# Performance work log

Measured on AMD Instinct MI355X. Metric: run time of the kernel, lower is better.

The kernel has to match this reference:

```python
import jax, jax.numpy as jnp
import numpy as np

N_NODES = 50000
N_EDGES = 800000
IN_CH = 384
HID = 128


def _gcn_conv(x, src, dst, W, b, n):
    # PyG GCNConv: h = x @ W; out[dst] += d^-1/2[src] * d^-1/2[dst] * h[src]; out += b
    h = x @ W  # [N, out_ch]
    deg = jax.ops.segment_sum(jnp.ones(src.shape, dtype=h.dtype), dst, num_segments=n)
    dinv = jnp.where(deg > 0, jax.lax.rsqrt(jnp.maximum(deg, 1.0)), 0.0)
    norm = dinv[src] * dinv[dst]  # [E]
    out = jax.ops.segment_sum(h[src] * norm[:, None], dst, num_segments=n)
    return out + b


def setup_inputs() -> dict:
    key = jax.random.key(0)
    k_x, k_e, k1, k2, k3, k4 = jax.random.split(key, 6)
    x = jax.random.normal(k_x, (N_NODES, IN_CH), dtype=jnp.float32)
    edge_index = jax.random.randint(k_e, (2, N_EDGES), 0, N_NODES, dtype=jnp.int64)
    s1 = 1.0 / np.sqrt(IN_CH)
    s2 = 1.0 / np.sqrt(HID)
    W1 = jax.random.uniform(k1, (IN_CH, HID), jnp.float32, -s1, s1)
    b1 = jnp.zeros((HID,), jnp.float32)
    W2 = jax.random.uniform(k2, (HID, HID), jnp.float32, -s2, s2)
    b2 = jnp.zeros((HID,), jnp.float32)
    return {"x": x, "edge_index": edge_index, "W1": W1, "b1": b1, "W2": W2, "b2": b2}


def reference(x, edge_index, W1, b1, W2, b2):
    n = x.shape[0]
    loops = jnp.arange(n, dtype=edge_index.dtype)
    src = jnp.concatenate([edge_index[0], loops])  # add_self_loops
    dst = jnp.concatenate([edge_index[1], loops])
    h = _gcn_conv(x, src, dst, W1, b1, n)
    h = jax.nn.relu(h)  # dropout is identity in eval mode
    out = _gcn_conv(h, src, dst, W2, b2, n)
    return out
```

## Files before the change

### kernel.cpp

```cpp
#include <hip/hip_runtime.h>
#include <hip/hip_fp16.h>

#define NN 50000
#define NE 800000
#define C_IN 384
#define C_HID 128
#define NB 196
#define CHK 128
#define ECH 6250
#define NBKT 128
#define BSTR 392

typedef __attribute__((ext_vector_type(8))) short short8;
typedef __attribute__((ext_vector_type(4))) float f32x4;
typedef __attribute__((ext_vector_type(4))) unsigned short us4;

__device__ __forceinline__ ushort f2bf(float x) {
    uint u = __float_as_uint(x);
    uint r = (u + 0x7fffu + ((u >> 16) & 1u)) >> 16;
    return (ushort)r;
}
__device__ __forceinline__ float bf2f(ushort b) { return __uint_as_float(((uint)b) << 16); }

__global__ __launch_bounds__(256) void k_dinv(const int* __restrict__ cnt,
                                              float* __restrict__ dinv) {
    int i = blockIdx.x * 256 + threadIdx.x;
    if (i < NN) dinv[i] = rsqrtf((float)cnt[i] + 1.0f);
}

__global__ __launch_bounds__(256) void k_bsum(const int* __restrict__ cnt,
                                              int* __restrict__ bsum) {
    __shared__ int part[256];
    const int tid = threadIdx.x;
    const int i = blockIdx.x * 256 + tid;
    part[tid] = (i < NN) ? cnt[i] : 0;
    __syncthreads();
#pragma unroll
    for (int off = 128; off > 0; off >>= 1) {
        if (tid < off) part[tid] += part[tid + off];
        __syncthreads();
    }
    if (tid == 0) bsum[blockIdx.x] = part[0];
}

__global__ __launch_bounds__(256) void k_sbs(const int* __restrict__ bsum,
                                             int* __restrict__ bpre) {
    __shared__ int part[256];
    const int t = threadIdx.x;
    part[t] = (t < NB) ? bsum[t] : 0;
    __syncthreads();
#pragma unroll
    for (int off = 1; off < 256; off <<= 1) {
        int v = (t >= off) ? part[t - off] : 0;
        __syncthreads();
        part[t] += v;
        __syncthreads();
    }
    if (t < NB) bpre[t] = (t == 0) ? 0 : part[t - 1];
}

__global__ __launch_bounds__(256) void k_write(const int* __restrict__ cnt,
                                               const int* __restrict__ bpre,
                                               int* __restrict__ rowptr) {
    __shared__ int part[256];
    const int t = threadIdx.x;
    const int i = blockIdx.x * 256 + t;
    const int v = (i < NN) ? cnt[i] : 0;
    part[t] = v;
    __syncthreads();
#pragma unroll
    for (int off = 1; off < 256; off <<= 1) {
        int u = (t >= off) ? part[t - off] : 0;
        __syncthreads();
        part[t] += u;
        __syncthreads();
    }
    if (i < NN) {
        const int excl = bpre[blockIdx.x] + part[t] - v;
        rowptr[i] = excl;
        if (i == NN - 1) rowptr[NN] = excl + v;
    }
}

__global__ __launch_bounds__(256) void k_hist(const int* __restrict__ dst,
                                              int* __restrict__ histT) {
    __shared__ int h[NBKT];
    const int tid = threadIdx.x;
    if (tid < NBKT) h[tid] = 0;
    __syncthreads();
    const int base = blockIdx.x * ECH;
    for (int i = base + tid; i < base + ECH; i += 256)
        atomicAdd(&h[(uint)dst[i] / BSTR], 1);
    __syncthreads();
    if (tid < NBKT) histT[tid * CHK + blockIdx.x] = h[tid];
}

__global__ __launch_bounds__(1024) void k_hscan(const int* __restrict__ histT,
                                                int* __restrict__ histS) {
    __shared__ int part[1024];
    const int t = threadIdx.x;
    const int base = t * 16;
    int loc[16];
    int s = 0;
#pragma unroll
    for (int i = 0; i < 16; ++i) {
        loc[i] = histT[base + i];
        s += loc[i];
    }
    part[t] = s;
    __syncthreads();
    for (int off = 1; off < 1024; off <<= 1) {
        int v = (t >= off) ? part[t - off] : 0;
        __syncthreads();
        part[t] += v;
        __syncthreads();
    }
    int run = (t == 0) ? 0 : part[t - 1];
#pragma unroll
    for (int i = 0; i < 16; ++i) {
        histS[base + i] = run;
        run += loc[i];
    }
}

__global__ __launch_bounds__(256) void k_binscat(const int* __restrict__ src,
                                                 const int* __restrict__ dst,
                                                 const int* __restrict__ histS,
                                                 uint2* __restrict__ mid) {
    __shared__ int cur[NBKT];
    const int tid = threadIdx.x;
    if (tid < NBKT) cur[tid] = histS[tid * CHK + blockIdx.x];
    __syncthreads();
    const int base = blockIdx.x * ECH;
    for (int i = base + tid; i < base + ECH; i += 256) {
        const int s = src[i];
        const int d = dst[i];
        const int p = atomicAdd(&cur[(uint)d / BSTR], 1);
        mid[p] = make_uint2((uint)d, (uint)s << 16);
    }
}

__global__ __launch_bounds__(256) void k_bcnt(const uint2* __restrict__ mid,
                                              const int* __restrict__ histS,
                                              int* __restrict__ cnt) {
    __shared__ int cur[BSTR];
    const int tid = threadIdx.x;
    const int b = blockIdx.x;
    for (int j = tid; j < BSTR; j += 256) cur[j] = 0;
    __syncthreads();
    const int lo = histS[b * CHK];
    const int hi = (b < NBKT - 1) ? histS[(b + 1) * CHK] : NE;
    for (int e = lo + tid; e < hi; e += 256)
        atomicAdd(&cur[mid[e].x - (uint)b * BSTR], 1);
    __syncthreads();
    for (int j = tid; j < BSTR; j += 256) {
        const int idx = b * BSTR + j;
        if (idx < NN) cnt[idx] = cur[j];
    }
}

__global__ __launch_bounds__(256) void k_binfill(const uint2* __restrict__ mid,
                                                 const int* __restrict__ histS,
                                                 const int* __restrict__ rowptr,
                                                 const float* __restrict__ dinv,
                                                 uint* __restrict__ csr) {
    __shared__ int cur[BSTR];
    __shared__ float sdv[BSTR];
    const int tid = threadIdx.x;
    const int b = blockIdx.x;
    for (int j = tid; j < BSTR; j += 256) {
        const int idx = b * BSTR + j;
        cur[j] = (idx < NN) ? rowptr[idx] : 0;
        sdv[j] = (idx < NN) ? dinv[idx] : 0.f;
    }
    __syncthreads();
    const int lo = histS[b * CHK];
    const int hi = (b < NBKT - 1) ? histS[(b + 1) * CHK] : NE;
    for (int e = lo + tid; e < hi; e += 256) {
        const uint2 u = mid[e];
        const int j = u.x - (uint)b * BSTR;
        const float norm = dinv[u.y >> 16] * sdv[j];
        const int p = atomicAdd(&cur[j], 1);
        csr[p] = u.y | __half_as_ushort(__float2half(norm));
    }
}

__global__ __launch_bounds__(256) void k_wconv(const float* __restrict__ W,
                                               ushort* __restrict__ Wt,
                                               int K) {
    int i = blockIdx.x * 256 + threadIdx.x;
    if (i < K * C_HID) {
        int k = i >> 7, n = i & 127;
        float w = W[i];
        ushort h = f2bf(w);
        ushort l = f2bf(w - bf2f(h));
        int blk = k >> 6, khalf = (k >> 5) & 1, kq = (k >> 3) & 3, j = k & 7;
        int t = n >> 4, fr = n & 15, lane = kq * 16 + fr;
        size_t off = (size_t)blk * 16384 + (size_t)((khalf * 8 + t) * 64 + lane) * 8 + j;
        Wt[off] = h;
        Wt[off + 8192] = l;
    }
}

template <bool IN_RELU_BIAS, bool OUT_BIAS>
__global__ __launch_bounds__(256, 4) void k_gemm_mfma(const float* __restrict__ X,
                                                      const ushort* __restrict__ Wt,
                                                      const float* __restrict__ bin,
                                                      const float* __restrict__ bout,
                                                      const float* __restrict__ dinv,
                                                      ushort* __restrict__ out_main,
                                                      float* __restrict__ out_self,
                                                      int K) {
    const int tid = threadIdx.x;
    const int bm = blockIdx.x * 32;
    const int wv = tid >> 6;
    const int lane = tid & 63;
    const int fr = lane & 15;
    const int kq = lane >> 4;
    const int g = wv >> 1;
    const int ch = wv & 1;

    int row = bm + g * 16 + fr;
    if (row >= NN) row = NN - 1;
    const float* xrow = X + (size_t)row * K + kq * 8;
    const short8* Wt8 = (const short8*)Wt;

    f32x4 acc[4];
#pragma unroll
    for (int t = 0; t < 4; ++t) acc[t] = (f32x4){0.f, 0.f, 0.f, 0.f};

    float4 xa0 = *(const float4*)(xrow);
    float4 xa1 = *(const float4*)(xrow + 4);
    float4 xb0 = *(const float4*)(xrow + 32);
    float4 xb1 = *(const float4*)(xrow + 36);

    for (int k0 = 0; k0 < K; k0 += 64) {
        const short8* gB = Wt8 + (size_t)(k0 >> 6) * 2048;
        short8 b_h0[4], b_l0[4], b_h1[4], b_l1[4];
#pragma unroll
        for (int t = 0; t < 4; ++t) {
            const int tt = ch * 4 + t;
            b_h0[t] = gB[tt * 64 + lane];
            b_l0[t] = gB[1024 + tt * 64 + lane];
            b_h1[t] = gB[(8 + tt) * 64 + lane];
            b_l1[t] = gB[1024 + (8 + tt) * 64 + lane];
        }

        float xv[16] = {xa0.x, xa0.y, xa0.z, xa0.w, xa1.x, xa1.y, xa1.z, xa1.w,
                        xb0.x, xb0.y, xb0.z, xb0.w, xb1.x, xb1.y, xb1.z, xb1.w};
        if (IN_RELU_BIAS) {
            const float* bp = bin + k0 + kq * 8;
            float4 b0 = *(const float4*)(bp);
            float4 b1 = *(const float4*)(bp + 4);
            float4 b2 = *(const float4*)(bp + 32);
            float4 b3 = *(const float4*)(bp + 36);
            const float bb[16] = {b0.x, b0.y, b0.z, b0.w, b1.x, b1.y, b1.z, b1.w,
                                  b2.x, b2.y, b2.z, b2.w, b3.x, b3.y, b3.z, b3.w};
#pragma unroll
            for (int j = 0; j < 16; ++j) xv[j] = fmaxf(xv[j] + bb[j], 0.f);
        }
        union { ushort u[8]; short8 v; } ah0, al0, ah1, al1;
#pragma unroll
        for (int j = 0; j < 8; ++j) {
            uint u = __float_as_uint(xv[j]);
            ah0.u[j] = (ushort)(u >> 16);
            al0.u[j] = (ushort)(__float_as_uint(xv[j] - __uint_as_float(u & 0xffff0000u)) >> 16);
            uint w = __float_as_uint(xv[8 + j]);
            ah1.u[j] = (ushort)(w >> 16);
            al1.u[j] = (ushort)(__float_as_uint(xv[8 + j] - __uint_as_float(w & 0xffff0000u)) >> 16);
        }

        if (k0 + 64 < K) {
            const float* ap = xrow + k0 + 64;
            xa0 = *(const float4*)(ap);
            xa1 = *(const float4*)(ap + 4);
            xb0 = *(const float4*)(ap + 32);
            xb1 = *(const float4*)(ap + 36);
        }

#pragma unroll
        for (int t = 0; t < 4; ++t) {
            acc[t] = __builtin_amdgcn_mfma_f32_16x16x32_bf16(ah0.v, b_h0[t], acc[t], 0, 0, 0);
            acc[t] = __builtin_amdgcn_mfma_f32_16x16x32_bf16(ah0.v, b_l0[t], acc[t], 0, 0, 0);
            acc[t] = __builtin_amdgcn_mfma_f32_16x16x32_bf16(al0.v, b_h0[t], acc[t], 0, 0, 0);
            acc[t] = __builtin_amdgcn_mfma_f32_16x16x32_bf16(ah1.v, b_h1[t], acc[t], 0, 0, 0);
            acc[t] = __builtin_amdgcn_mfma_f32_16x16x32_bf16(ah1.v, b_l1[t], acc[t], 0, 0, 0);
            acc[t] = __builtin_amdgcn_mfma_f32_16x16x32_bf16(al1.v, b_h1[t], acc[t], 0, 0, 0);
        }
    }

#pragma unroll
    for (int r = 0; r < 4; ++r) {
        const int m = bm + g * 16 + kq * 4 + r;
        if (m < NN) {
            const float dv = dinv[m];
            const float d2 = dv * dv;
            ushort* om = out_main + (size_t)m * C_HID;
            float* os = out_self + (size_t)m * C_HID;
#pragma unroll
            for (int t = 0; t < 4; ++t) {
                const int n = (ch * 4 + t) * 16 + fr;
                const float v = acc[t][r];
                om[n] = f2bf(v);
                os[n] = v * d2 + (OUT_BIAS ? bout[n] : 0.f);
            }
        }
    }
}

__global__ __launch_bounds__(256) void k_gather(const ushort* __restrict__ h,
                                                const int* __restrict__ rowptr,
                                                const uint* __restrict__ csr,
                                                float* __restrict__ out) {
    const int tid = threadIdx.x;
    const int node = blockIdx.x * 8 + (tid >> 5);
    if (node >= NN) return;
    const int lane = tid & 31;
    const int c = lane * 4;
    const int beg = rowptr[node];
    const int end = rowptr[node + 1];

    float4 acc = *(const float4*)(out + (size_t)node * C_HID + c);

    for (int j0 = beg; j0 < end; j0 += 32) {
        const int n = end - j0;
        uint myE = 0;
        if (lane < n) myE = csr[j0 + lane];
        const int m = n < 32 ? n : 32;
        int jj = 0;
        for (; jj + 4 <= m; jj += 4) {
            const uint e0 = (uint)__shfl((int)myE, jj + 0, 32);
            const uint e1 = (uint)__shfl((int)myE, jj + 1, 32);
            const uint e2 = (uint)__shfl((int)myE, jj + 2, 32);
            const uint e3 = (uint)__shfl((int)myE, jj + 3, 32);
            const us4 u0 = *(const us4*)(h + (size_t)(e0 >> 16) * C_HID + c);
            const us4 u1 = *(const us4*)(h + (size_t)(e1 >> 16) * C_HID + c);
            const us4 u2 = *(const us4*)(h + (size_t)(e2 >> 16) * C_HID + c);
            const us4 u3 = *(const us4*)(h + (size_t)(e3 >> 16) * C_HID + c);
            const float n0 = __half2float(__ushort_as_half((ushort)(e0 & 0xffffu)));
            const float n1 = __half2float(__ushort_as_half((ushort)(e1 & 0xffffu)));
            const float n2 = __half2float(__ushort_as_half((ushort)(e2 & 0xffffu)));
            const float n3 = __half2float(__ushort_as_half((ushort)(e3 & 0xffffu)));
            acc.x = fmaf(bf2f(u0[0]), n0, acc.x);
            acc.y = fmaf(bf2f(u0[1]), n0, acc.y);
            acc.z = fmaf(bf2f(u0[2]), n0, acc.z);
            acc.w = fmaf(bf2f(u0[3]), n0, acc.w);
            acc.x = fmaf(bf2f(u1[0]), n1, acc.x);
            acc.y = fmaf(bf2f(u1[1]), n1, acc.y);
            acc.z = fmaf(bf2f(u1[2]), n1, acc.z);
            acc.w = fmaf(bf2f(u1[3]), n1, acc.w);
            acc.x = fmaf(bf2f(u2[0]), n2, acc.x);
            acc.y = fmaf(bf2f(u2[1]), n2, acc.y);
            acc.z = fmaf(bf2f(u2[2]), n2, acc.z);
            acc.w = fmaf(bf2f(u2[3]), n2, acc.w);
            acc.x = fmaf(bf2f(u3[0]), n3, acc.x);
            acc.y = fmaf(bf2f(u3[1]), n3, acc.y);
            acc.z = fmaf(bf2f(u3[2]), n3, acc.z);
            acc.w = fmaf(bf2f(u3[3]), n3, acc.w);
        }
        for (; jj < m; ++jj) {
            const uint ev = (uint)__shfl((int)myE, jj, 32);
            const us4 u = *(const us4*)(h + (size_t)(ev >> 16) * C_HID + c);
            const float nw = __half2float(__ushort_as_half((ushort)(ev & 0xffffu)));
            acc.x = fmaf(bf2f(u[0]), nw, acc.x);
            acc.y = fmaf(bf2f(u[1]), nw, acc.y);
            acc.z = fmaf(bf2f(u[2]), nw, acc.z);
            acc.w = fmaf(bf2f(u[3]), nw, acc.w);
        }
    }
    *(float4*)(out + (size_t)node * C_HID + c) = acc;
}

extern "C" void kernel_launch(void* const* d_in, const int* in_sizes, int n_in,
                              void* d_out, int out_size, void* d_ws, size_t ws_size,
                              hipStream_t stream) {
    const float* x = (const float*)d_in[0];
    const int* ei = (const int*)d_in[1];
    const float* W1 = (const float*)d_in[2];
    const float* b1 = (const float*)d_in[3];
    const float* W2 = (const float*)d_in[4];
    const float* b2 = (const float*)d_in[5];
    float* out = (float*)d_out;

    const int* src = ei;
    const int* dst = ei + NE;

    int* cnt = (int*)d_ws;
    int* rowptr = cnt + 50048;
    float* dinv = (float*)(rowptr + 50064);
    int* bsum = (int*)(dinv + 50048);
    int* bpre = bsum + 256;
    int* histT = bpre + 256;
    int* histS = histT + 16384;
    ushort* Wt1 = (ushort*)(histS + 16384);
    ushort* Wt2 = Wt1 + 98304;
    uint* csr = (uint*)(Wt2 + 32768);
    uint2* mid = (uint2*)(csr + NE);
    ushort* A_bf = (ushort*)(mid + NE);
    float* B = (float*)(A_bf + (size_t)NN * C_HID);

    k_wconv<<<(C_IN * C_HID + 255) / 256, 256, 0, stream>>>(W1, Wt1, C_IN);
    k_wconv<<<(C_HID * C_HID + 255) / 256, 256, 0, stream>>>(W2, Wt2, C_HID);
    k_hist<<<CHK, 256, 0, stream>>>(dst, histT);
    k_hscan<<<1, 1024, 0, stream>>>(histT, histS);
    k_binscat<<<CHK, 256, 0, stream>>>(src, dst, histS, mid);
    k_bcnt<<<NBKT, 256, 0, stream>>>(mid, histS, cnt);
    k_dinv<<<NB, 256, 0, stream>>>(cnt, dinv);
    k_bsum<<<NB, 256, 0, stream>>>(cnt, bsum);
    k_sbs<<<1, 256, 0, stream>>>(bsum, bpre);
    k_write<<<NB, 256, 0, stream>>>(cnt, bpre, rowptr);
    k_binfill<<<NBKT, 256, 0, stream>>>(mid, histS, rowptr, dinv, csr);

    const int gblocks = (NN + 31) / 32;
    const int agblocks = (NN + 7) / 8;
    k_gemm_mfma<false, false><<<gblocks, 256, 0, stream>>>(x, Wt1, nullptr, nullptr, dinv, A_bf, B, C_IN);
    k_gather<<<agblocks, 256, 0, stream>>>(A_bf, rowptr, csr, B);
    k_gemm_mfma<true, true><<<gblocks, 256, 0, stream>>>(B, Wt2, b1, b2, dinv, A_bf, out, C_HID);
    k_gather<<<agblocks, 256, 0, stream>>>(A_bf, rowptr, csr, out);
}
```

Before: 354.7 us.

## Stage GEMM weights and activations through double-buffered LDS with async loads

Rewrites the MFMA GEMM to use 512-thread blocks over 64 rows. Weight tiles are loaded asynchronously into double-buffered LDS with global_load_lds, and the X tile goes into swizzled LDS instead of each wave reading global memory directly. The K step shrinks to 32, the weight layout is re-packed to match, and the bias is staged in LDS. The goal is to share weight loads across waves and overlap the next tile's fetch with the MFMA work. The cost is per-step barriers, hand-placed waitcnts whose correctness depends on ordering, and lower occupancy from more LDS use.

```diff
diff --git a/kernel.cpp b/kernel.cpp
--- a/kernel.cpp
+++ b/kernel.cpp
@@ -22,6 +22,12 @@
 }
 __device__ __forceinline__ float bf2f(ushort b) { return __uint_as_float(((uint)b) << 16); }
 
+typedef __attribute__((address_space(1))) const unsigned int as1_uint;
+typedef __attribute__((address_space(3))) unsigned int as3_uint;
+__device__ __forceinline__ void gload16(const void* g, void* l) {
+    __builtin_amdgcn_global_load_lds((as1_uint*)g, (as3_uint*)l, 16, 0, 0);
+}
+
 __global__ __launch_bounds__(256) void k_dinv(const int* __restrict__ cnt,
                                               float* __restrict__ dinv) {
     int i = blockIdx.x * 256 + threadIdx.x;
@@ -194,98 +200,185 @@
         float w = W[i];
         ushort h = f2bf(w);
         ushort l = f2bf(w - bf2f(h));
-        int blk = k >> 6, khalf = (k >> 5) & 1, kq = (k >> 3) & 3, j = k & 7;
+        int blk = k >> 5, kq = (k >> 3) & 3, j = k & 7;
         int t = n >> 4, fr = n & 15, lane = kq * 16 + fr;
-        size_t off = (size_t)blk * 16384 + (size_t)((khalf * 8 + t) * 64 + lane) * 8 + j;
+        size_t off = ((size_t)blk * 1024 + t * 64 + lane) * 8 + j;
         Wt[off] = h;
-        Wt[off + 8192] = l;
-    }
-}
+        Wt[off + 4096] = l;
+    }
+}
+
+#define GEMM_BODY(KB, CUR, NXT, XOLD, XNEW)                                               \
+    {                                                                                     \
+        _Pragma("unroll")                                                                 \
+        for (int i_ = 0; i_ < 2; ++i_)                                                    \
+            gload16(Wt8 + (size_t)((KB) + 1) * 1024 + wv * 128 + i_ * 64 + lane,          \
+                    &WL[NXT][wv * 128 + i_ * 64]);                                        \
+        __builtin_amdgcn_sched_barrier(0);                                                \
+        XNEW = *(const float4*)(xsrc + ((KB) + 2) * 32);                                  \
+        *(float4*)(xdst[NXT]) = XOLD;                                                     \
+        const float* xb_ = &XL[CUR][ar * 32];                                             \
+        float4 xf0 = *(const float4*)(xb_ + ac0);                                         \
+        float4 xf1 = *(const float4*)(xb_ + ac1);                                         \
+        float xv[8] = {xf0.x, xf0.y, xf0.z, xf0.w, xf1.x, xf1.y, xf1.z, xf1.w};           \
+        if (IN_RELU_BIAS) {                                                               \
+            float4 b0 = *(const float4*)(&bias_lds[(KB) * 32 + kq * 8]);                  \
+            float4 b1 = *(const float4*)(&bias_lds[(KB) * 32 + kq * 8 + 4]);              \
+            const float bb[8] = {b0.x, b0.y, b0.z, b0.w, b1.x, b1.y, b1.z, b1.w};         \
+            _Pragma("unroll")                                                             \
+            for (int j_ = 0; j_ < 8; ++j_) xv[j_] = fmaxf(xv[j_] + bb[j_], 0.f);          \
+        }                                                                                 \
+        union { ushort u[8]; short8 v; } ah, al;                                          \
+        _Pragma("unroll")                                                                 \
+        for (int j_ = 0; j_ < 8; ++j_) {                                                  \
+            uint u_ = __float_as_uint(xv[j_]);                                            \
+            ah.u[j_] = (ushort)(u_ >> 16);                                                \
+            al.u[j_] = (ushort)(__float_as_uint(xv[j_] - __uint_as_float(u_ & 0xffff0000u)) >> 16); \
+        }                                                                                 \
+        __builtin_amdgcn_s_setprio(1);                                                    \
+        _Pragma("unroll")                                                                 \
+        for (int t_ = 0; t_ < 4; ++t_) {                                                  \
+            const int tt_ = ch * 4 + t_;                                                  \
+            const short8 wh_ = WL[CUR][tt_ * 64 + lane];                                  \
+            const short8 wl_ = WL[CUR][512 + tt_ * 64 + lane];                            \
+            acc[t_] = __builtin_amdgcn_mfma_f32_16x16x32_bf16(ah.v, wh_, acc[t_], 0, 0, 0); \
+            acc[t_] = __builtin_amdgcn_mfma_f32_16x16x32_bf16(ah.v, wl_, acc[t_], 0, 0, 0); \
+            acc[t_] = __builtin_amdgcn_mfma_f32_16x16x32_bf16(al.v, wh_, acc[t_], 0, 0, 0); \
+        }                                                                                 \
+        __builtin_amdgcn_s_setprio(0);                                                    \
+        __builtin_amdgcn_sched_barrier(0);                                                \
+        asm volatile("s_waitcnt vmcnt(1) lgkmcnt(0)" ::: "memory");                       \
+        __builtin_amdgcn_sched_barrier(0);                                                \
+        __builtin_amdgcn_s_barrier();                                                     \
+    }
 
 template <bool IN_RELU_BIAS, bool OUT_BIAS>
-__global__ __launch_bounds__(256, 4) void k_gemm_mfma(const float* __restrict__ X,
-                                                      const ushort* __restrict__ Wt,
-                                                      const float* __restrict__ bin,
-                                                      const float* __restrict__ bout,
-                                                      const float* __restrict__ dinv,
-                                                      ushort* __restrict__ out_main,
-                                                      float* __restrict__ out_self,
-                                                      int K) {
-    const int tid = threadIdx.x;
-    const int bm = blockIdx.x * 32;
+__global__ __launch_bounds__(512) void k_gemm_mfma(const float* __restrict__ X,
+                                                   const ushort* __restrict__ Wt,
+                                                   const float* __restrict__ bin,
+                                                   const float* __restrict__ bout,
+                                                   const float* __restrict__ dinv,
+                                                   ushort* __restrict__ out_main,
+                                                   float* __restrict__ out_self,
+                                                   int K) {
+    __shared__ short8 WL[2][1024];
+    __shared__ float XL[2][2048];
+    __shared__ float bias_lds[128];
+
+    const int tid = threadIdx.x;
+    const int bm = blockIdx.x * 64;
     const int wv = tid >> 6;
     const int lane = tid & 63;
     const int fr = lane & 15;
     const int kq = lane >> 4;
     const int g = wv >> 1;
     const int ch = wv & 1;
-
-    int row = bm + g * 16 + fr;
-    if (row >= NN) row = NN - 1;
-    const float* xrow = X + (size_t)row * K + kq * 8;
+    const int NK = K >> 5;
+
     const short8* Wt8 = (const short8*)Wt;
 
+    const int xr = tid >> 3;
+    const int xc16 = tid & 7;
+    int xrow = bm + xr;
+    if (xrow >= NN) xrow = NN - 1;
+    const float* xsrc = X + (size_t)xrow * K + xc16 * 4;
+    float* xdst[2] = {&XL[0][xr * 32 + ((xc16 ^ (xr & 7)) * 4)],
+                      &XL[1][xr * 32 + ((xc16 ^ (xr & 7)) * 4)]};
+
+    const int ar = g * 16 + fr;
+    const int ac0 = ((2 * kq) ^ (ar & 7)) * 4;
+    const int ac1 = ((2 * kq + 1) ^ (ar & 7)) * 4;
+
     f32x4 acc[4];
 #pragma unroll
     for (int t = 0; t < 4; ++t) acc[t] = (f32x4){0.f, 0.f, 0.f, 0.f};
 
-    float4 xa0 = *(const float4*)(xrow);
-    float4 xa1 = *(const float4*)(xrow + 4);
-    float4 xb0 = *(const float4*)(xrow + 32);
-    float4 xb1 = *(const float4*)(xrow + 36);
-
-    for (int k0 = 0; k0 < K; k0 += 64) {
-        const short8* gB = Wt8 + (size_t)(k0 >> 6) * 2048;
-        short8 b_h0[4], b_l0[4], b_h1[4], b_l1[4];
-#pragma unroll
-        for (int t = 0; t < 4; ++t) {
-            const int tt = ch * 4 + t;
-            b_h0[t] = gB[tt * 64 + lane];
-            b_l0[t] = gB[1024 + tt * 64 + lane];
-            b_h1[t] = gB[(8 + tt) * 64 + lane];
-            b_l1[t] = gB[1024 + (8 + tt) * 64 + lane];
-        }
-
-        float xv[16] = {xa0.x, xa0.y, xa0.z, xa0.w, xa1.x, xa1.y, xa1.z, xa1.w,
-                        xb0.x, xb0.y, xb0.z, xb0.w, xb1.x, xb1.y, xb1.z, xb1.w};
+    if (IN_RELU_BIAS && tid < 128) bias_lds[tid] = bin[tid];
+
+#pragma unroll
+    for (int i_ = 0; i_ < 2; ++i_)
+        gload16(Wt8 + (size_t)wv * 128 + i_ * 64 + lane, &WL[0][wv * 128 + i_ * 64]);
+    __builtin_amdgcn_sched_barrier(0);
+    float4 xA = *(const float4*)(xsrc);
+    float4 xB = *(const float4*)(xsrc + 32);
+    *(float4*)(xdst[0]) = xA;
+    xA = xB;
+    asm volatile("s_waitcnt lgkmcnt(0)" ::: "memory");
+    __builtin_amdgcn_sched_barrier(0);
+    __builtin_amdgcn_s_barrier();
+
+    for (int kb = 0; kb < NK - 2; kb += 2) {
+        GEMM_BODY(kb, 0, 1, xA, xB);
+        GEMM_BODY(kb + 1, 1, 0, xB, xA);
+    }
+
+    {
+        const int KB = NK - 2;
+#pragma unroll
+        for (int i_ = 0; i_ < 2; ++i_)
+            gload16(Wt8 + (size_t)(KB + 1) * 1024 + wv * 128 + i_ * 64 + lane,
+                    &WL[1][wv * 128 + i_ * 64]);
+        *(float4*)(xdst[1]) = xA;
+        const float* xb_ = &XL[0][ar * 32];
+        float4 xf0 = *(const float4*)(xb_ + ac0);
+        float4 xf1 = *(const float4*)(xb_ + ac1);
+        float xv[8] = {xf0.x, xf0.y, xf0.z, xf0.w, xf1.x, xf1.y, xf1.z, xf1.w};
         if (IN_RELU_BIAS) {
-            const float* bp = bin + k0 + kq * 8;
-            float4 b0 = *(const float4*)(bp);
-            float4 b1 = *(const float4*)(bp + 4);
-            float4 b2 = *(const float4*)(bp + 32);
-            float4 b3 = *(const float4*)(bp + 36);
-            const float bb[16] = {b0.x, b0.y, b0.z, b0.w, b1.x, b1.y, b1.z, b1.w,
-                                  b2.x, b2.y, b2.z, b2.w, b3.x, b3.y, b3.z, b3.w};
-#pragma unroll
-            for (int j = 0; j < 16; ++j) xv[j] = fmaxf(xv[j] + bb[j], 0.f);
-        }
-        union { ushort u[8]; short8 v; } ah0, al0, ah1, al1;
-#pragma unroll
-        for (int j = 0; j < 8; ++j) {
-            uint u = __float_as_uint(xv[j]);
-            ah0.u[j] = (ushort)(u >> 16);
-            al0.u[j] = (ushort)(__float_as_uint(xv[j] - __uint_as_float(u & 0xffff0000u)) >> 16);
-            uint w = __float_as_uint(xv[8 + j]);
-            ah1.u[j] = (ushort)(w >> 16);
-            al1.u[j] = (ushort)(__float_as_uint(xv[8 + j] - __uint_as_float(w & 0xffff0000u)) >> 16);
-        }
-
-        if (k0 + 64 < K) {
-            const float* ap = xrow + k0 + 64;
-            xa0 = *(const float4*)(ap);
-            xa1 = *(const float4*)(ap + 4);
-            xb0 = *(const float4*)(ap + 32);
-            xb1 = *(const float4*)(ap + 36);
-        }
-
-#pragma unroll
-        for (int t = 0; t < 4; ++t) {
-            acc[t] = __builtin_amdgcn_mfma_f32_16x16x32_bf16(ah0.v, b_h0[t], acc[t], 0, 0, 0);
-            acc[t] = __builtin_amdgcn_mfma_f32_16x16x32_bf16(ah0.v, b_l0[t], acc[t], 0, 0, 0);
-            acc[t] = __builtin_amdgcn_mfma_f32_16x16x32_bf16(al0.v, b_h0[t], acc[t], 0, 0, 0);
-            acc[t] = __builtin_amdgcn_mfma_f32_16x16x32_bf16(ah1.v, b_h1[t], acc[t], 0, 0, 0);
-            acc[t] = __builtin_amdgcn_mfma_f32_16x16x32_bf16(ah1.v, b_l1[t], acc[t], 0, 0, 0);
-            acc[t] = __builtin_amdgcn_mfma_f32_16x16x32_bf16(al1.v, b_h1[t], acc[t], 0, 0, 0);
+            float4 b0 = *(const float4*)(&bias_lds[KB * 32 + kq * 8]);
+            float4 b1 = *(const float4*)(&bias_lds[KB * 32 + kq * 8 + 4]);
+            const float bb[8] = {b0.x, b0.y, b0.z, b0.w, b1.x, b1.y, b1.z, b1.w};
+#pragma unroll
+            for (int j_ = 0; j_ < 8; ++j_) xv[j_] = fmaxf(xv[j_] + bb[j_], 0.f);
+        }
+        union { ushort u[8]; short8 v; } ah, al;
+#pragma unroll
+        for (int j_ = 0; j_ < 8; ++j_) {
+            uint u_ = __float_as_uint(xv[j_]);
+            ah.u[j_] = (ushort)(u_ >> 16);
+            al.u[j_] = (ushort)(__float_as_uint(xv[j_] - __uint_as_float(u_ & 0xffff0000u)) >> 16);
+        }
+#pragma unroll
+        for (int t_ = 0; t_ < 4; ++t_) {
+            const int tt_ = ch * 4 + t_;
+            const short8 wh_ = WL[0][tt_ * 64 + lane];
+            const short8 wl_ = WL[0][512 + tt_ * 64 + lane];
+            acc[t_] = __builtin_amdgcn_mfma_f32_16x16x32_bf16(ah.v, wh_, acc[t_], 0, 0, 0);
+            acc[t_] = __builtin_amdgcn_mfma_f32_16x16x32_bf16(ah.v, wl_, acc[t_], 0, 0, 0);
+            acc[t_] = __builtin_amdgcn_mfma_f32_16x16x32_bf16(al.v, wh_, acc[t_], 0, 0, 0);
+        }
+        __builtin_amdgcn_sched_barrier(0);
+        asm volatile("s_waitcnt vmcnt(0) lgkmcnt(0)" ::: "memory");
+        __builtin_amdgcn_sched_barrier(0);
+        __builtin_amdgcn_s_barrier();
+    }
+    {
+        const int KB = NK - 1;
+        const float* xb_ = &XL[1][ar * 32];
+        float4 xf0 = *(const float4*)(xb_ + ac0);
+        float4 xf1 = *(const float4*)(xb_ + ac1);
+        float xv[8] = {xf0.x, xf0.y, xf0.z, xf0.w, xf1.x, xf1.y, xf1.z, xf1.w};
+        if (IN_RELU_BIAS) {
+            float4 b0 = *(const float4*)(&bias_lds[KB * 32 + kq * 8]);
+            float4 b1 = *(const float4*)(&bias_lds[KB * 32 + kq * 8 + 4]);
+            const float bb[8] = {b0.x, b0.y, b0.z, b0.w, b1.x, b1.y, b1.z, b1.w};
+#pragma unroll
+            for (int j_ = 0; j_ < 8; ++j_) xv[j_] = fmaxf(xv[j_] + bb[j_], 0.f);
+        }
+        union { ushort u[8]; short8 v; } ah, al;
+#pragma unroll
+        for (int j_ = 0; j_ < 8; ++j_) {
+            uint u_ = __float_as_uint(xv[j_]);
+            ah.u[j_] = (ushort)(u_ >> 16);
+            al.u[j_] = (ushort)(__float_as_uint(xv[j_] - __uint_as_float(u_ & 0xffff0000u)) >> 16);
+        }
+#pragma unroll
+        for (int t_ = 0; t_ < 4; ++t_) {
+            const int tt_ = ch * 4 + t_;
+            const short8 wh_ = WL[1][tt_ * 64 + lane];
+            const short8 wl_ = WL[1][512 + tt_ * 64 + lane];
+            acc[t_] = __builtin_amdgcn_mfma_f32_16x16x32_bf16(ah.v, wh_, acc[t_], 0, 0, 0);
+            acc[t_] = __builtin_amdgcn_mfma_f32_16x16x32_bf16(ah.v, wl_, acc[t_], 0, 0, 0);
+            acc[t_] = __builtin_amdgcn_mfma_f32_16x16x32_bf16(al.v, wh_, acc[t_], 0, 0, 0);
         }
     }
 
@@ -411,10 +504,10 @@
     k_write<<<NB, 256, 0, stream>>>(cnt, bpre, rowptr);
     k_binfill<<<NBKT, 256, 0, stream>>>(mid, histS, rowptr, dinv, csr);
 
-    const int gblocks = (NN + 31) / 32;
+    const int gblocks = (NN + 63) / 64;
     const int agblocks = (NN + 7) / 8;
-    k_gemm_mfma<false, false><<<gblocks, 256, 0, stream>>>(x, Wt1, nullptr, nullptr, dinv, A_bf, B, C_IN);
+    k_gemm_mfma<false, false><<<gblocks, 512, 0, stream>>>(x, Wt1, nullptr, nullptr, dinv, A_bf, B, C_IN);
     k_gather<<<agblocks, 256, 0, stream>>>(A_bf, rowptr, csr, B);
-    k_gemm_mfma<true, true><<<gblocks, 256, 0, stream>>>(B, Wt2, b1, b2, dinv, A_bf, out, C_HID);
+    k_gemm_mfma<true, true><<<gblocks, 512, 0, stream>>>(B, Wt2, b1, b2, dinv, A_bf, out, C_HID);
     k_gather<<<agblocks, 256, 0, stream>>>(A_bf, rowptr, csr, out);
 }
```

Measured after the change: 309.8 us. 12.6% less time.

## Stage GEMM weights and split-bf16 activations through double-buffered LDS

Applied to the files above, without the earlier changes.

The dense GEMM kernels now use 512-thread blocks covering 64 rows. Weights are loaded into double-buffered LDS with direct global-to-LDS loads, and each activation tile is converted once into hi/lo bf16 parts and stored in swizzled LDS, instead of every wave reloading weights from global memory and converting its own X slice. The K loop steps by 32 with software pipelining, explicit waitcnt and barriers, and raised MFMA priority, so loads should overlap compute and redundant weight traffic drops. The cost is more LDS use, a barrier every K step, and more complex, fragile synchronisation.

```diff
diff --git a/kernel.cpp b/kernel.cpp
--- a/kernel.cpp
+++ b/kernel.cpp
@@ -22,6 +22,12 @@
 }
 __device__ __forceinline__ float bf2f(ushort b) { return __uint_as_float(((uint)b) << 16); }
 
+typedef __attribute__((address_space(1))) const unsigned int as1_uint;
+typedef __attribute__((address_space(3))) unsigned int as3_uint;
+__device__ __forceinline__ void gload16(const void* g, void* l) {
+    __builtin_amdgcn_global_load_lds((as1_uint*)g, (as3_uint*)l, 16, 0, 0);
+}
+
 __global__ __launch_bounds__(256) void k_dinv(const int* __restrict__ cnt,
                                               float* __restrict__ dinv) {
     int i = blockIdx.x * 256 + threadIdx.x;
@@ -194,100 +200,178 @@
         float w = W[i];
         ushort h = f2bf(w);
         ushort l = f2bf(w - bf2f(h));
-        int blk = k >> 6, khalf = (k >> 5) & 1, kq = (k >> 3) & 3, j = k & 7;
+        int blk = k >> 5, kq = (k >> 3) & 3, j = k & 7;
         int t = n >> 4, fr = n & 15, lane = kq * 16 + fr;
-        size_t off = (size_t)blk * 16384 + (size_t)((khalf * 8 + t) * 64 + lane) * 8 + j;
+        size_t off = ((size_t)blk * 1024 + t * 64 + lane) * 8 + j;
         Wt[off] = h;
-        Wt[off + 8192] = l;
-    }
-}
+        Wt[off + 4096] = l;
+    }
+}
+
+#define STAGE_X(NXT, XOLD, KB1)                                                          \
+    {                                                                                    \
+        float xs0 = XOLD.x, xs1 = XOLD.y, xs2 = XOLD.z, xs3 = XOLD.w;                    \
+        if (IN_RELU_BIAS) {                                                              \
+            float4 bq = *(const float4*)(&bias_lds[(KB1) * 32 + (tid & 7) * 4]);         \
+            xs0 = fmaxf(xs0 + bq.x, 0.f);                                                \
+            xs1 = fmaxf(xs1 + bq.y, 0.f);                                                \
+            xs2 = fmaxf(xs2 + bq.z, 0.f);                                                \
+            xs3 = fmaxf(xs3 + bq.w, 0.f);                                                \
+        }                                                                                \
+        const uint u0 = __float_as_uint(xs0), u1 = __float_as_uint(xs1);                 \
+        const uint u2 = __float_as_uint(xs2), u3 = __float_as_uint(xs3);                 \
+        const uint h01 = (u0 >> 16) | (u1 & 0xffff0000u);                                \
+        const uint h23 = (u2 >> 16) | (u3 & 0xffff0000u);                                \
+        const uint l0 = __float_as_uint(xs0 - __uint_as_float(u0 & 0xffff0000u));        \
+        const uint l1 = __float_as_uint(xs1 - __uint_as_float(u1 & 0xffff0000u));        \
+        const uint l2 = __float_as_uint(xs2 - __uint_as_float(u2 & 0xffff0000u));        \
+        const uint l3 = __float_as_uint(xs3 - __uint_as_float(u3 & 0xffff0000u));        \
+        const uint l01 = (l0 >> 16) | (l1 & 0xffff0000u);                                \
+        const uint l23 = (l2 >> 16) | (l3 & 0xffff0000u);                                \
+        *(uint2*)&XLh[NXT][xw] = make_uint2(h01, h23);                                   \
+        *(uint2*)&XLl[NXT][xw] = make_uint2(l01, l23);                                   \
+    }
+
+#define GEMM_BODY(KB, CUR, NXT, XOLD, XNEW)                                              \
+    {                                                                                    \
+        _Pragma("unroll")                                                                \
+        for (int i_ = 0; i_ < 2; ++i_)                                                   \
+            gload16(Wt8 + (size_t)((KB) + 1) * 1024 + wv * 128 + i_ * 64 + lane,         \
+                    &WL[NXT][wv * 128 + i_ * 64]);                                       \
+        __builtin_amdgcn_sched_barrier(0);                                               \
+        XNEW = *(const float4*)(xsrc + ((KB) + 2) * 32);                                 \
+        const short8 ahh = *(const short8*)&XLh[CUR][axh];                               \
+        const short8 all = *(const short8*)&XLl[CUR][axh];                               \
+        const short8 wh0 = WL[CUR][(tb + 0) * 64 + lane];                                \
+        const short8 wl0 = WL[CUR][512 + (tb + 0) * 64 + lane];                          \
+        const short8 wh1 = WL[CUR][(tb + 1) * 64 + lane];                                \
+        const short8 wl1 = WL[CUR][512 + (tb + 1) * 64 + lane];                          \
+        const short8 wh2 = WL[CUR][(tb + 2) * 64 + lane];                                \
+        const short8 wl2 = WL[CUR][512 + (tb + 2) * 64 + lane];                          \
+        const short8 wh3 = WL[CUR][(tb + 3) * 64 + lane];                                \
+        const short8 wl3 = WL[CUR][512 + (tb + 3) * 64 + lane];                          \
+        STAGE_X(NXT, XOLD, (KB) + 1);                                                    \
+        __builtin_amdgcn_s_setprio(1);                                                   \
+        acc[0] = __builtin_amdgcn_mfma_f32_16x16x32_bf16(ahh, wh0, acc[0], 0, 0, 0);     \
+        acc[0] = __builtin_amdgcn_mfma_f32_16x16x32_bf16(ahh, wl0, acc[0], 0, 0, 0);     \
+        acc[0] = __builtin_amdgcn_mfma_f32_16x16x32_bf16(all, wh0, acc[0], 0, 0, 0);     \
+        acc[1] = __builtin_amdgcn_mfma_f32_16x16x32_bf16(ahh, wh1, acc[1], 0, 0, 0);     \
+        acc[1] = __builtin_amdgcn_mfma_f32_16x16x32_bf16(ahh, wl1, acc[1], 0, 0, 0);     \
+        acc[1] = __builtin_amdgcn_mfma_f32_16x16x32_bf16(all, wh1, acc[1], 0, 0, 0);     \
+        acc[2] = __builtin_amdgcn_mfma_f32_16x16x32_bf16(ahh, wh2, acc[2], 0, 0, 0);     \
+        acc[2] = __builtin_amdgcn_mfma_f32_16x16x32_bf16(ahh, wl2, acc[2], 0, 0, 0);     \
+        acc[2] = __builtin_amdgcn_mfma_f32_16x16x32_bf16(all, wh2, acc[2], 0, 0, 0);     \
+        acc[3] = __builtin_amdgcn_mfma_f32_16x16x32_bf16(ahh, wh3, acc[3], 0, 0, 0);     \
+        acc[3] = __builtin_amdgcn_mfma_f32_16x16x32_bf16(ahh, wl3, acc[3], 0, 0, 0);     \
+        acc[3] = __builtin_amdgcn_mfma_f32_16x16x32_bf16(all, wh3, acc[3], 0, 0, 0);     \
+        __builtin_amdgcn_s_setprio(0);                                                   \
+        __builtin_amdgcn_sched_barrier(0);                                               \
+        asm volatile("s_waitcnt vmcnt(1) lgkmcnt(0)" ::: "memory");                      \
+        __builtin_amdgcn_sched_barrier(0);                                               \
+        __builtin_amdgcn_s_barrier();                                                    \
+    }
+
+#define GEMM_TAIL(KB, CUR, DO_MFMA_ONLY)                                                 \
+    {                                                                                    \
+        const short8 ahh = *(const short8*)&XLh[CUR][axh];                               \
+        const short8 all = *(const short8*)&XLl[CUR][axh];                               \
+        const short8 wh0 = WL[CUR][(tb + 0) * 64 + lane];                                \
+        const short8 wl0 = WL[CUR][512 + (tb + 0) * 64 + lane];                          \
+        const short8 wh1 = WL[CUR][(tb + 1) * 64 + lane];                                \
+        const short8 wl1 = WL[CUR][512 + (tb + 1) * 64 + lane];                          \
+        const short8 wh2 = WL[CUR][(tb + 2) * 64 + lane];                                \
+        const short8 wl2 = WL[CUR][512 + (tb + 2) * 64 + lane];                          \
+        const short8 wh3 = WL[CUR][(tb + 3) * 64 + lane];                                \
+        const short8 wl3 = WL[CUR][512 + (tb + 3) * 64 + lane];                          \
+        acc[0] = __builtin_amdgcn_mfma_f32_16x16x32_bf16(ahh, wh0, acc[0], 0, 0, 0);     \
+        acc[0] = __builtin_amdgcn_mfma_f32_16x16x32_bf16(ahh, wl0, acc[0], 0, 0, 0);     \
+        acc[0] = __builtin_amdgcn_mfma_f32_16x16x32_bf16(all, wh0, acc[0], 0, 0, 0);     \
+        acc[1] = __builtin_amdgcn_mfma_f32_16x16x32_bf16(ahh, wh1, acc[1], 0, 0, 0);     \
+        acc[1] = __builtin_amdgcn_mfma_f32_16x16x32_bf16(ahh, wl1, acc[1], 0, 0, 0);     \
+        acc[1] = __builtin_amdgcn_mfma_f32_16x16x32_bf16(all, wh1, acc[1], 0, 0, 0);     \
+        acc[2] = __builtin_amdgcn_mfma_f32_16x16x32_bf16(ahh, wh2, acc[2], 0, 0, 0);     \
+        acc[2] = __builtin_amdgcn_mfma_f32_16x16x32_bf16(ahh, wl2, acc[2], 0, 0, 0);     \
+        acc[2] = __builtin_amdgcn_mfma_f32_16x16x32_bf16(all, wh2, acc[2], 0, 0, 0);     \
+        acc[3] = __builtin_amdgcn_mfma_f32_16x16x32_bf16(ahh, wh3, acc[3], 0, 0, 0);     \
+        acc[3] = __builtin_amdgcn_mfma_f32_16x16x32_bf16(ahh, wl3, acc[3], 0, 0, 0);     \
+        acc[3] = __builtin_amdgcn_mfma_f32_16x16x32_bf16(all, wh3, acc[3], 0, 0, 0);     \
+    }
 
 template <bool IN_RELU_BIAS, bool OUT_BIAS>
-__global__ __launch_bounds__(256, 4) void k_gemm_mfma(const float* __restrict__ X,
-                                                      const ushort* __restrict__ Wt,
-                                                      const float* __restrict__ bin,
-                                                      const float* __restrict__ bout,
-                                                      const float* __restrict__ dinv,
-                                                      ushort* __restrict__ out_main,
-                                                      float* __restrict__ out_self,
-                                                      int K) {
-    const int tid = threadIdx.x;
-    const int bm = blockIdx.x * 32;
+__global__ __launch_bounds__(512) void k_gemm_mfma(const float* __restrict__ X,
+                                                   const ushort* __restrict__ Wt,
+                                                   const float* __restrict__ bin,
+                                                   const float* __restrict__ bout,
+                                                   const float* __restrict__ dinv,
+                                                   ushort* __restrict__ out_main,
+                                                   float* __restrict__ out_self,
+                                                   int K) {
+    __shared__ short8 WL[2][1024];
+    __shared__ ushort XLh[2][2048];
+    __shared__ ushort XLl[2][2048];
+    __shared__ float bias_lds[128];
+
+    const int tid = threadIdx.x;
+    const int bm = blockIdx.x * 64;
     const int wv = tid >> 6;
     const int lane = tid & 63;
     const int fr = lane & 15;
     const int kq = lane >> 4;
     const int g = wv >> 1;
     const int ch = wv & 1;
-
-    int row = bm + g * 16 + fr;
-    if (row >= NN) row = NN - 1;
-    const float* xrow = X + (size_t)row * K + kq * 8;
+    const int tb = ch * 4;
+    const int NK = K >> 5;
+
     const short8* Wt8 = (const short8*)Wt;
 
+    const int xr = tid >> 3;
+    const int xc8 = tid & 7;
+    int xrow = bm + xr;
+    if (xrow >= NN) xrow = NN - 1;
+    const float* xsrc = X + (size_t)xrow * K + xc8 * 4;
+    const int xw = xr * 32 + (((xc8 >> 1) ^ (xr & 3)) << 3) + ((xc8 & 1) << 2);
+
+    const int ar = g * 16 + fr;
+    const int axh = ar * 32 + ((kq ^ (ar & 3)) << 3);
+
     f32x4 acc[4];
 #pragma unroll
     for (int t = 0; t < 4; ++t) acc[t] = (f32x4){0.f, 0.f, 0.f, 0.f};
 
-    float4 xa0 = *(const float4*)(xrow);
-    float4 xa1 = *(const float4*)(xrow + 4);
-    float4 xb0 = *(const float4*)(xrow + 32);
-    float4 xb1 = *(const float4*)(xrow + 36);
-
-    for (int k0 = 0; k0 < K; k0 += 64) {
-        const short8* gB = Wt8 + (size_t)(k0 >> 6) * 2048;
-        short8 b_h0[4], b_l0[4], b_h1[4], b_l1[4];
-#pragma unroll
-        for (int t = 0; t < 4; ++t) {
-            const int tt = ch * 4 + t;
-            b_h0[t] = gB[tt * 64 + lane];
-            b_l0[t] = gB[1024 + tt * 64 + lane];
-            b_h1[t] = gB[(8 + tt) * 64 + lane];
-            b_l1[t] = gB[1024 + (8 + tt) * 64 + lane];
-        }
-
-        float xv[16] = {xa0.x, xa0.y, xa0.z, xa0.w, xa1.x, xa1.y, xa1.z, xa1.w,
-                        xb0.x, xb0.y, xb0.z, xb0.w, xb1.x, xb1.y, xb1.z, xb1.w};
-        if (IN_RELU_BIAS) {
-            const float* bp = bin + k0 + kq * 8;
-            float4 b0 = *(const float4*)(bp);
-            float4 b1 = *(const float4*)(bp + 4);
-            float4 b2 = *(const float4*)(bp + 32);
-            float4 b3 = *(const float4*)(bp + 36);
-            const float bb[16] = {b0.x, b0.y, b0.z, b0.w, b1.x, b1.y, b1.z, b1.w,
-                                  b2.x, b2.y, b2.z, b2.w, b3.x, b3.y, b3.z, b3.w};
-#pragma unroll
-            for (int j = 0; j < 16; ++j) xv[j] = fmaxf(xv[j] + bb[j], 0.f);
-        }
-        union { ushort u[8]; short8 v; } ah0, al0, ah1, al1;
-#pragma unroll
-        for (int j = 0; j < 8; ++j) {
-            uint u = __float_as_uint(xv[j]);
-            ah0.u[j] = (ushort)(u >> 16);
-            al0.u[j] = (ushort)(__float_as_uint(xv[j] - __uint_as_float(u & 0xffff0000u)) >> 16);
-            uint w = __float_as_uint(xv[8 + j]);
-            ah1.u[j] = (ushort)(w >> 16);
-            al1.u[j] = (ushort)(__float_as_uint(xv[8 + j] - __uint_as_float(w & 0xffff0000u)) >> 16);
-        }
-
-        if (k0 + 64 < K) {
-            const float* ap = xrow + k0 + 64;
-            xa0 = *(const float4*)(ap);
-            xa1 = *(const float4*)(ap + 4);
-            xb0 = *(const float4*)(ap + 32);
-            xb1 = *(const float4*)(ap + 36);
-        }
-
-#pragma unroll
-        for (int t = 0; t < 4; ++t) {
-            acc[t] = __builtin_amdgcn_mfma_f32_16x16x32_bf16(ah0.v, b_h0[t], acc[t], 0, 0, 0);
-            acc[t] = __builtin_amdgcn_mfma_f32_16x16x32_bf16(ah0.v, b_l0[t], acc[t], 0, 0, 0);
-            acc[t] = __builtin_amdgcn_mfma_f32_16x16x32_bf16(al0.v, b_h0[t], acc[t], 0, 0, 0);
-            acc[t] = __builtin_amdgcn_mfma_f32_16x16x32_bf16(ah1.v, b_h1[t], acc[t], 0, 0, 0);
-            acc[t] = __builtin_amdgcn_mfma_f32_16x16x32_bf16(ah1.v, b_l1[t], acc[t], 0, 0, 0);
-            acc[t] = __builtin_amdgcn_mfma_f32_16x16x32_bf16(al1.v, b_h1[t], acc[t], 0, 0, 0);
-        }
-    }
+    if (IN_RELU_BIAS && tid < 128) bias_lds[tid] = bin[tid];
+
+#pragma unroll
+    for (int i_ = 0; i_ < 2; ++i_)
+        gload16(Wt8 + (size_t)wv * 128 + i_ * 64 + lane, &WL[0][wv * 128 + i_ * 64]);
+    __builtin_amdgcn_sched_barrier(0);
+    float4 xA = *(const float4*)(xsrc);
+    float4 xB = *(const float4*)(xsrc + 32);
+    asm volatile("s_waitcnt lgkmcnt(0)" ::: "memory");
+    __builtin_amdgcn_s_barrier();
+    STAGE_X(0, xA, 0);
+    xA = xB;
+    asm volatile("s_waitcnt lgkmcnt(0)" ::: "memory");
+    __builtin_amdgcn_s_barrier();
+
+    for (int kb = 0; kb < NK - 2; kb += 2) {
+        GEMM_BODY(kb, 0, 1, xA, xB);
+        GEMM_BODY(kb + 1, 1, 0, xB, xA);
+    }
+
+    {
+        const int KB = NK - 2;
+#pragma unroll
+        for (int i_ = 0; i_ < 2; ++i_)
+            gload16(Wt8 + (size_t)(KB + 1) * 1024 + wv * 128 + i_ * 64 + lane,
+                    &WL[1][wv * 128 + i_ * 64]);
+        STAGE_X(1, xA, KB + 1);
+        GEMM_TAIL(KB, 0, 0);
+        __builtin_amdgcn_sched_barrier(0);
+        asm volatile("s_waitcnt vmcnt(0) lgkmcnt(0)" ::: "memory");
+        __builtin_amdgcn_sched_barrier(0);
+        __builtin_amdgcn_s_barrier();
+    }
+    GEMM_TAIL(NK - 1, 1, 1);
 
 #pragma unroll
     for (int r = 0; r < 4; ++r) {
@@ -411,10 +495,10 @@
     k_write<<<NB, 256, 0, stream>>>(cnt, bpre, rowptr);
     k_binfill<<<NBKT, 256, 0, stream>>>(mid, histS, rowptr, dinv, csr);
 
-    const int gblocks = (NN + 31) / 32;
+    const int gblocks = (NN + 63) / 64;
     const int agblocks = (NN + 7) / 8;
-    k_gemm_mfma<false, false><<<gblocks, 256, 0, stream>>>(x, Wt1, nullptr, nullptr, dinv, A_bf, B, C_IN);
+    k_gemm_mfma<false, false><<<gblocks, 512, 0, stream>>>(x, Wt1, nullptr, nullptr, dinv, A_bf, B, C_IN);
     k_gather<<<agblocks, 256, 0, stream>>>(A_bf, rowptr, csr, B);
-    k_gemm_mfma<true, true><<<gblocks, 256, 0, stream>>>(B, Wt2, b1, b2, dinv, A_bf, out, C_HID);
+    k_gemm_mfma<true, true><<<gblocks, 512, 0, stream>>>(B, Wt2, b1, b2, dinv, A_bf, out, C_HID);
     k_gather<<<agblocks, 256, 0, stream>>>(A_bf, rowptr, csr, out);
 }
```

Result: faster. 300.7 us (-15.2%).
